# Performance work log

Measured on AMD Instinct MI355X. Metric: run time of the kernel, lower is better.

## Reference

```python
import jax, jax.numpy as jnp
import numpy as np

HID, NH_FULL, K, GAMMA = 768, 12, 9, 2
HD = HID // NH_FULL            # 64
NH = NH_FULL // GAMMA          # 6
RH = HD * NH                   # 384 reduced hidden dim
OUT_HALF = HID // 2            # 384
B, S = 8, 1024


def setup_inputs() -> dict:
    key0 = jax.random.key(0)
    ks = jax.random.split(key0, 20)
    r = lambda i, shape, sc=0.02: (jax.random.normal(ks[i], shape, dtype=jnp.float32) * sc)
    inp = {
        'query': jax.random.normal(ks[0], (B, S, HID), dtype=jnp.float32),
        'mask': jnp.ones((B, 1, 1, S), dtype=jnp.int32),
        # q/k/v projections: hidden -> reduced
        'Wq': r(1, (HID, RH)), 'bq': jnp.zeros((RH,), jnp.float32),
        'Wk': r(2, (HID, RH)), 'bk': jnp.zeros((RH,), jnp.float32),
        'Wv': r(3, (HID, RH)), 'bv': jnp.zeros((RH,), jnp.float32),
        # depthwise separable conv: depthwise [HID,1,K] + pointwise [RH,HID]
        'dw_w': r(4, (HID, 1, K), 0.1), 'dw_b': jnp.zeros((HID,), jnp.float32),
        'pw_w': r(5, (RH, HID)), 'pw_b': jnp.zeros((RH,), jnp.float32),
        # self-attn output proj: reduced -> hidden//2
        'Wsa': r(6, (RH, OUT_HALF)), 'bsa': jnp.zeros((OUT_HALF,), jnp.float32),
        # dynamic kernel layer: reduced -> K*NH
        'Wdk': r(7, (RH, K * NH)), 'bdk': jnp.zeros((K * NH,), jnp.float32),
        # dynamic attn output proj: reduced -> hidden//2
        'Wda': r(8, (RH, OUT_HALF)), 'bda': jnp.zeros((OUT_HALF,), jnp.float32),
    }
    # self_attn=True requires query==key==value
    inp['key'] = inp['query']
    inp['value'] = inp['query']
    return inp


def _forward(query, key, value, mask, Wq, bq, Wk, bk, Wv, bv,
             dw_w, dw_b, pw_w, pw_b, Wsa, bsa, Wdk, bdk, Wda, bda):
    b, s, _ = query.shape
    q = query @ Wq + bq          # [B,S,RH]
    k = key @ Wk + bk
    v = value @ Wv + bv

    # ---- depthwise separable conv over key (seq axis), 'same' padding ----
    key_t = jnp.transpose(key, (0, 2, 1))  # [B,HID,S]
    dw = jax.lax.conv_general_dilated(
        key_t, dw_w, window_strides=(1,), padding=[(K // 2, K // 2)],
        feature_group_count=HID, dimension_numbers=('NCH', 'OIH', 'NCH'))
    dw = dw + dw_b[None, :, None]          # [B,HID,S]
    ks_feat = jnp.einsum('bhs,rh->bsr', dw, pw_w) + pw_b  # [B,S,RH]

    # ---- standard multi-head self-attention branch ----
    def split(x):  # [B,S,RH] -> [B,NH,S,HD]
        return x.reshape(b, s, NH, HD).transpose(0, 2, 1, 3)
    qh, kh, vh = split(q), split(k), split(v)
    scores = jnp.einsum('bhqd,bhkd->bhqk', qh, kh) / jnp.sqrt(jnp.float32(HD))
    scores = jnp.where(mask == 0, jnp.float32(-jnp.inf), scores)
    attn_wts = jax.nn.softmax(scores, axis=-1)             # [B,NH,S,S]
    attn_out = jnp.einsum('bhqk,bhkd->bhqd', attn_wts, vh)
    attn_out = attn_out.transpose(0, 2, 1, 3).reshape(b, s, RH)
    self_out = attn_out @ Wsa + bsa                         # [B,S,HID//2]

    # ---- span dynamic conv attention branch ----
    # unfold v into sliding windows: expanded[b,s,h,d,k] = v_pad[b, s+k, h*HD+d]
    v_pad = jnp.pad(v, ((0, 0), (K // 2, K // 2), (0, 0)))  # [B,S+K-1,RH]
    windows = jnp.stack([v_pad[:, i:i + s] for i in range(K)], axis=-1)  # [B,S,RH,K]
    windows = windows.reshape(b, s, NH, HD, K)
    dyn_logits = (q * ks_feat) @ Wdk + bdk                  # [B,S,K*NH]
    dyn_kernel = jax.nn.softmax(dyn_logits.reshape(b, s, NH, K), axis=-1)
    dyn_out = jnp.einsum('bshdk,bshk->bshd', windows, dyn_kernel).reshape(b, s, RH)
    dyn_out = dyn_out @ Wda + bda                           # [B,S,HID//2]

    return attn_wts, jnp.concatenate([self_out, dyn_out], axis=-1)


def reference(query, key, value, mask, Wq, bq, Wk, bk, Wv, bv,
              dw_w, dw_b, pw_w, pw_b, Wsa, bsa, Wdk, bdk, Wda, bda):
    return _forward(query, key, value, mask, Wq, bq, Wk, bk, Wv, bv,
                    dw_w, dw_b, pw_w, pw_b, Wsa, bsa, Wdk, bdk, Wda, bda)
```

## Files before the change

kernel.cpp:

```cpp
#include <hip/hip_runtime.h>
#include <math.h>

#define B 8
#define S 1024
#define HID 768
#define RH 384
#define NH 6
#define HD 64
#define KW 9
#define KNH 54
#define OUTHALF 384
#define QLD 1152
#define EXPSCALE 0.18033688f

typedef __attribute__((ext_vector_type(8))) short short8;
typedef __attribute__((ext_vector_type(4))) float f32x4;

#define SWZ(r, c) (((r) << 6) + ((c) ^ (((r) & 7) << 3)))

__device__ __forceinline__ ushort f2bf(float x) {
    unsigned u = __float_as_uint(x);
    u += 0x7FFF + ((u >> 16) & 1);
    return (ushort)(u >> 16);
}
__device__ __forceinline__ float bf2f(ushort u) {
    return __uint_as_float(((unsigned)u) << 16);
}
__device__ __forceinline__ short8 cvt8(const float* p) {
    short8 r;
    #pragma unroll
    for (int i = 0; i < 8; i++) r[i] = (short)f2bf(p[i]);
    return r;
}

__device__ __forceinline__ void gld16(const ushort* g, ushort* l) {
    __builtin_amdgcn_global_load_lds(
        (const __attribute__((address_space(1))) void*)g,
        (__attribute__((address_space(3))) void*)l,
        16, 0, 0);
}

__global__ __launch_bounds__(256) void cvt_dw_fused(
    const float* __restrict__ query, const float* __restrict__ dw_w,
    const float* __restrict__ dw_b, ushort* __restrict__ Xbf,
    ushort* __restrict__ dwout)
{
    int idx = blockIdx.x*256 + threadIdx.x;
    if (idx >= B*S*(HID/8)) return;
    int c0 = (idx % (HID/8))*8;
    int s  = (idx / (HID/8)) % S;
    int b  = idx / ((HID/8)*S);

    float ctr[8];
    *(float4*)&ctr[0] = *(const float4*)(query + ((size_t)b*S + s)*HID + c0);
    *(float4*)&ctr[4] = *(const float4*)(query + ((size_t)b*S + s)*HID + c0 + 4);
    *(short8*)(Xbf + ((size_t)b*S + s)*HID + c0) = cvt8(ctr);

    float acc[8];
    *(float4*)&acc[0] = *(const float4*)(dw_b + c0);
    *(float4*)&acc[4] = *(const float4*)(dw_b + c0 + 4);
    #pragma unroll
    for (int kk = 0; kk < KW; kk++) {
        int sp = s + kk - KW/2;
        if (sp >= 0 && sp < S) {
            float row[8];
            *(float4*)&row[0] = *(const float4*)(query + ((size_t)b*S + sp)*HID + c0);
            *(float4*)&row[4] = *(const float4*)(query + ((size_t)b*S + sp)*HID + c0 + 4);
            #pragma unroll
            for (int j = 0; j < 8; j++)
                acc[j] += row[j] * dw_w[(c0+j)*KW + kk];
        }
    }
    *(short8*)(dwout + ((size_t)b*S + s)*HID + c0) = cvt8(acc);
}

__global__ __launch_bounds__(256) void prep_weights(
    const float* __restrict__ Wq, const float* __restrict__ Wk, const float* __restrict__ Wv,
    const float* __restrict__ bq, const float* __restrict__ bk, const float* __restrict__ bv,
    const float* __restrict__ pw_w, const float* __restrict__ Wsa,
    const float* __restrict__ Wda, const float* __restrict__ Wdk,
    ushort* __restrict__ WqkvT, ushort* __restrict__ pw_bf,
    ushort* __restrict__ WsaT, ushort* __restrict__ WdaT, ushort* __restrict__ WdkT,
    float* __restrict__ bqkv)
{
    int i = blockIdx.x*256 + threadIdx.x;
    if (i < 884736) {
        int n = i / 768, kk = i % 768;
        int w = n / 384, nn = n % 384;
        const float* W = (w == 0) ? Wq : (w == 1) ? Wk : Wv;
        WqkvT[i] = f2bf(W[kk*384 + nn]);
        return;
    }
    i -= 884736;
    if (i < 294912) { pw_bf[i] = f2bf(pw_w[i]); return; }
    i -= 294912;
    if (i < 147456) {
        int n = i / 384, kk = i % 384;
        WsaT[i] = f2bf(Wsa[kk*384 + n]);
        return;
    }
    i -= 147456;
    if (i < 147456) {
        int n = i / 384, kk = i % 384;
        WdaT[i] = f2bf(Wda[kk*384 + n]);
        return;
    }
    i -= 147456;
    if (i < 49152) {
        int n = i / 384, kk = i % 384;
        WdkT[i] = (n < KNH) ? f2bf(Wdk[kk*KNH + n]) : (ushort)0;
        return;
    }
    i -= 49152;
    if (i < 1152) {
        bqkv[i] = (i < 384) ? bq[i] : (i < 768) ? bk[i-384] : bv[i-768];
    }
}

template<bool OUTBF>
__global__ __launch_bounds__(256) void gemm_mfma(
    const ushort* __restrict__ A, const ushort* __restrict__ Bt,
    const float* __restrict__ bias, void* __restrict__ Cout,
    int N, int Kd, int ldc)
{
    __shared__ __attribute__((aligned(16))) ushort As[128*32];
    __shared__ __attribute__((aligned(16))) ushort Bs[128*32];
    const int t = threadIdx.x;
    const int wave = t >> 6, lane = t & 63;
    const int lr = lane & 15, lg = lane >> 4;
    const int wr = wave >> 1, wc = wave & 1;
    const int bm = blockIdx.y * 128, bn = blockIdx.x * 128;

    f32x4 acc[4][4] = {};
    const int srow = t >> 2, sseg = t & 3;
    const int cs = sseg ^ (srow & 3);
    const int swz = lg ^ (lr & 3);

    const ushort* Asrc0 = A + (size_t)(bm + srow)*Kd + cs*8;
    const ushort* Asrc1 = A + (size_t)(bm + 64 + srow)*Kd + cs*8;
    const ushort* Bsrc0 = Bt + (size_t)(bn + srow)*Kd + cs*8;
    const ushort* Bsrc1 = Bt + (size_t)(bn + 64 + srow)*Kd + cs*8;
    ushort* Adst0 = &As[srow*32 + sseg*8];
    ushort* Adst1 = &As[(64 + srow)*32 + sseg*8];
    ushort* Bdst0 = &Bs[srow*32 + sseg*8];
    ushort* Bdst1 = &Bs[(64 + srow)*32 + sseg*8];

    for (int k0 = 0; k0 < Kd; k0 += 32) {
        gld16(Asrc0 + k0, Adst0);
        gld16(Asrc1 + k0, Adst1);
        gld16(Bsrc0 + k0, Bdst0);
        gld16(Bsrc1 + k0, Bdst1);
        __syncthreads();
        short8 af[4], bfr[4];
        #pragma unroll
        for (int m = 0; m < 4; m++)
            af[m] = *(const short8*)&As[(wr*64 + m*16 + lr)*32 + swz*8];
        #pragma unroll
        for (int n = 0; n < 4; n++)
            bfr[n] = *(const short8*)&Bs[(wc*64 + n*16 + lr)*32 + swz*8];
        #pragma unroll
        for (int m = 0; m < 4; m++)
            #pragma unroll
            for (int n = 0; n < 4; n++)
                acc[m][n] = __builtin_amdgcn_mfma_f32_16x16x32_bf16(af[m], bfr[n], acc[m][n], 0, 0, 0);
        __syncthreads();
    }

    #pragma unroll
    for (int m = 0; m < 4; m++) {
        #pragma unroll
        for (int n = 0; n < 4; n++) {
            int gcol = bn + wc*64 + n*16 + lr;
            if (gcol >= N) continue;
            float bz = bias[gcol];
            #pragma unroll
            for (int r = 0; r < 4; r++) {
                size_t grow = bm + wr*64 + m*16 + lg*4 + r;
                float val = acc[m][n][r] + bz;
                if (OUTBF) ((ushort*)Cout)[grow*ldc + gcol] = f2bf(val);
                else       ((float*)Cout)[grow*ldc + gcol] = val;
            }
        }
    }
}

template<bool OUTBF, bool DUAL>
__global__ __launch_bounds__(256) void gemm64(
    const ushort* __restrict__ A0, const ushort* __restrict__ Bt0,
    const float* __restrict__ bias0, void* __restrict__ C0,
    const ushort* __restrict__ A1, const ushort* __restrict__ Bt1,
    const float* __restrict__ bias1,
    int N, int Kd, int ldc)
{
    __shared__ __attribute__((aligned(16))) ushort As[64*32];
    __shared__ __attribute__((aligned(16))) ushort Bs[64*32];
    const ushort* A  = (DUAL && blockIdx.z) ? A1 : A0;
    const ushort* Bt = (DUAL && blockIdx.z) ? Bt1 : Bt0;
    const float* bias = (DUAL && blockIdx.z) ? bias1 : bias0;
    const int coff = (DUAL && blockIdx.z) ? OUTHALF : 0;

    const int t = threadIdx.x;
    const int wave = t >> 6, lane = t & 63;
    const int lr = lane & 15, lg = lane >> 4;
    const int wr = wave >> 1, wc = wave & 1;
    const int bm = blockIdx.y * 64, bn = blockIdx.x * 64;

    f32x4 acc[2][2] = {};
    const int srow = t >> 2, sseg = t & 3;
    const int cs = sseg ^ (srow & 3);
    const int swz = lg ^ (lr & 3);
    const ushort* Asrc = A + (size_t)(bm + srow)*Kd + cs*8;
    const ushort* Bsrc = Bt + (size_t)(bn + srow)*Kd + cs*8;
    ushort* Adst = &As[srow*32 + sseg*8];
    ushort* Bdst = &Bs[srow*32 + sseg*8];

    for (int k0 = 0; k0 < Kd; k0 += 32) {
        gld16(Asrc + k0, Adst);
        gld16(Bsrc + k0, Bdst);
        __syncthreads();
        short8 af[2], bfr[2];
        #pragma unroll
        for (int m = 0; m < 2; m++)
            af[m] = *(const short8*)&As[(wr*32 + m*16 + lr)*32 + swz*8];
        #pragma unroll
        for (int n = 0; n < 2; n++)
            bfr[n] = *(const short8*)&Bs[(wc*32 + n*16 + lr)*32 + swz*8];
        #pragma unroll
        for (int m = 0; m < 2; m++)
            #pragma unroll
            for (int n = 0; n < 2; n++)
                acc[m][n] = __builtin_amdgcn_mfma_f32_16x16x32_bf16(af[m], bfr[n], acc[m][n], 0, 0, 0);
        __syncthreads();
    }

    #pragma unroll
    for (int m = 0; m < 2; m++) {
        #pragma unroll
        for (int n = 0; n < 2; n++) {
            int gcol = bn + wc*32 + n*16 + lr;
            if (gcol >= N) continue;
            float bz = bias[gcol];
            #pragma unroll
            for (int r = 0; r < 4; r++) {
                size_t grow = bm + wr*32 + m*16 + lg*4 + r;
                float val = acc[m][n][r] + bz;
                if (OUTBF) ((ushort*)C0)[grow*ldc + gcol + coff] = f2bf(val);
                else       ((float*)C0)[grow*ldc + gcol + coff] = val;
            }
        }
    }
}

__global__ __launch_bounds__(64) void gemm_qksdk(
    const ushort* __restrict__ qkv, const ushort* __restrict__ ksf,
    const ushort* __restrict__ WdkT, const float* __restrict__ bdk,
    float* __restrict__ dynlog)
{
    const int lane = threadIdx.x;
    const int lr = lane & 15, lg = lane >> 4;
    const int r0 = blockIdx.x * 16;
    const int row = r0 + lr;

    f32x4 acc[4] = {};
    for (int ks = 0; ks < RH/32; ks++) {
        int k0 = ks*32 + lg*8;
        short8 qv = *(const short8*)(qkv + (size_t)row*QLD + k0);
        short8 kv = *(const short8*)(ksf + (size_t)row*RH + k0);
        short8 afr;
        #pragma unroll
        for (int j = 0; j < 8; j++)
            afr[j] = (short)f2bf(bf2f((ushort)qv[j]) * bf2f((ushort)kv[j]));
        #pragma unroll
        for (int t4 = 0; t4 < 4; t4++) {
            short8 bfr = *(const short8*)(WdkT + (size_t)(t4*16 + lr)*RH + k0);
            acc[t4] = __builtin_amdgcn_mfma_f32_16x16x32_bf16(afr, bfr, acc[t4], 0, 0, 0);
        }
    }
    #pragma unroll
    for (int t4 = 0; t4 < 4; t4++) {
        int n = t4*16 + lr;
        if (n >= KNH) continue;
        float bz = bdk[n];
        #pragma unroll
        for (int r = 0; r < 4; r++)
            dynlog[(size_t)(r0 + lg*4 + r)*KNH + n] = acc[t4][r] + bz;
    }
}

__global__ __launch_bounds__(256) void attn_scores(
    const ushort* __restrict__ qkv, const int* __restrict__ mask,
    ushort* __restrict__ Praw, float* __restrict__ invbuf)
{
    __shared__ __attribute__((aligned(16))) ushort Ks[2][64*64];
    __shared__ __attribute__((aligned(16))) ushort Ps[4][16*64];

    const int b = blockIdx.z, h = blockIdx.y, q0 = blockIdx.x * 64;
    const int t = threadIdx.x;
    const int wave = t >> 6, lane = t & 63;
    const int lr = lane & 15, lg = lane >> 4;

    const ushort* qrow = qkv + (size_t)(b*S + q0 + wave*16 + lr)*QLD + h*HD;
    short8 aQ0 = *(const short8*)(qrow + lg*8);
    short8 aQ1 = *(const short8*)(qrow + 32 + lg*8);

    const int srow = t >> 2, sseg = t & 3;
    const int* mrow = mask + b*S;
    const ushort* krbase = qkv + RH + (size_t)(b*S + srow)*QLD + h*HD + sseg*16;
    ushort* Psw = &Ps[wave][0];
    const size_t prow0 = (size_t)(b*NH + h)*S + q0 + wave*16;

    float lsum[4] = {0.f, 0.f, 0.f, 0.f};

    {
        short8 k0v = *(const short8*)(krbase);
        short8 k1v = *(const short8*)(krbase + 8);
        *(short8*)&Ks[0][SWZ(srow, sseg*16)]     = k0v;
        *(short8*)&Ks[0][SWZ(srow, sseg*16 + 8)] = k1v;
    }
    __syncthreads();
    int cur = 0;

    for (int kc = 0; kc < S; kc += 64) {
        short8 nk0, nk1;
        if (kc + 64 < S) {
            const ushort* kr = krbase + (size_t)(kc + 64)*QLD;
            nk0 = *(const short8*)(kr);
            nk1 = *(const short8*)(kr + 8);
        }
        #pragma unroll
        for (int t4 = 0; t4 < 4; t4++) {
            short8 b0 = *(const short8*)&Ks[cur][SWZ(t4*16 + lr, lg*8)];
            short8 b1 = *(const short8*)&Ks[cur][SWZ(t4*16 + lr, 32 + lg*8)];
            f32x4 c = {0.f, 0.f, 0.f, 0.f};
            c = __builtin_amdgcn_mfma_f32_16x16x32_bf16(aQ0, b0, c, 0, 0, 0);
            c = __builtin_amdgcn_mfma_f32_16x16x32_bf16(aQ1, b1, c, 0, 0, 0);
            float add = mrow[kc + t4*16 + lr] ? 0.f : -1e30f;
            #pragma unroll
            for (int r = 0; r < 4; r++) {
                float p = exp2f(c[r]*EXPSCALE + add);
                lsum[r] += p;
                Psw[SWZ(lg*4 + r, t4*16 + lr)] = f2bf(p);
            }
        }
        {
            int row = lane & 15, seg = lane >> 4;
            short8 p0 = *(const short8*)&Psw[SWZ(row, seg*16)];
            short8 p1 = *(const short8*)&Psw[SWZ(row, seg*16 + 8)];
            ushort* gp = Praw + (prow0 + row)*S + kc + seg*16;
            *(short8*)gp       = p0;
            *(short8*)(gp + 8) = p1;
        }
        if (kc + 64 < S) {
            *(short8*)&Ks[cur^1][SWZ(srow, sseg*16)]     = nk0;
            *(short8*)&Ks[cur^1][SWZ(srow, sseg*16 + 8)] = nk1;
        }
        __syncthreads();
        cur ^= 1;
    }

    #pragma unroll
    for (int r = 0; r < 4; r++) {
        #pragma unroll
        for (int off = 1; off < 16; off <<= 1)
            lsum[r] += __shfl_xor(lsum[r], off, 16);
    }
    if (lr == 0) {
        #pragma unroll
        for (int r = 0; r < 4; r++)
            invbuf[prow0 + lg*4 + r] = 1.f / lsum[r];
    }
}

__global__ __launch_bounds__(256) void attn_pv(
    const ushort* __restrict__ qkv, const ushort* __restrict__ Praw,
    const float* __restrict__ invbuf, float* __restrict__ out0,
    ushort* __restrict__ attnbf)
{
    __shared__ __attribute__((aligned(16))) ushort Pt[2][64*64];
    __shared__ __attribute__((aligned(16))) ushort Vt[2][64*64];

    const int b = blockIdx.z, h = blockIdx.y, q0 = blockIdx.x * 64;
    const int t = threadIdx.x;
    const int wave = t >> 6, lane = t & 63;
    const int lr = lane & 15, lg = lane >> 4;
    const int srow = t >> 2, sseg = t & 3;

    const size_t rbase = (size_t)(b*NH + h)*S + q0;
    const ushort* prbase = Praw + (rbase + srow)*S + sseg*16;
    const ushort* vbase  = qkv + 2*RH + (size_t)b*S*QLD + h*HD + srow;

    const float inv_c = invbuf[rbase + wave*16 + lr];
    float inv_o[4];
    #pragma unroll
    for (int r = 0; r < 4; r++) inv_o[r] = invbuf[rbase + wave*16 + lg*4 + r];

    {
        short8 p0 = *(const short8*)(prbase);
        short8 p1 = *(const short8*)(prbase + 8);
        ushort vb[16];
        #pragma unroll
        for (int i = 0; i < 16; i++)
            vb[i] = vbase[(size_t)(sseg*16 + i)*QLD];
        *(short8*)&Pt[0][SWZ(srow, sseg*16)]     = p0;
        *(short8*)&Pt[0][SWZ(srow, sseg*16 + 8)] = p1;
        *(short8*)&Vt[0][SWZ(srow, sseg*16)]     = *(short8*)&vb[0];
        *(short8*)&Vt[0][SWZ(srow, sseg*16 + 8)] = *(short8*)&vb[8];
    }
    __syncthreads();
    int cur = 0;

    f32x4 o[4] = {};
    const size_t orow = (rbase + wave*16 + lr)*(size_t)S;

    for (int kc = 0; kc < S; kc += 64) {
        short8 np0, np1;
        ushort vb[16];
        if (kc + 64 < S) {
            np0 = *(const short8*)(prbase + kc + 64);
            np1 = *(const short8*)(prbase + kc + 72);
            const ushort* vp = vbase + (size_t)(kc + 64)*QLD;
            #pragma unroll
            for (int i = 0; i < 16; i++)
                vb[i] = vp[(size_t)(sseg*16 + i)*QLD];
        }

        #pragma unroll
        for (int kh = 0; kh < 2; kh++) {
            short8 pa = *(const short8*)&Pt[cur][SWZ(wave*16 + lr, kh*32 + lg*8)];
            float pf[8];
            #pragma unroll
            for (int j = 0; j < 8; j++) pf[j] = bf2f((ushort)pa[j]) * inv_c;
            float* op = out0 + orow + kc + kh*32 + lg*8;
            __builtin_nontemporal_store(*(f32x4*)&pf[0], (f32x4*)op);
            __builtin_nontemporal_store(*(f32x4*)&pf[4], (f32x4*)(op + 4));
            #pragma unroll
            for (int dt = 0; dt < 4; dt++) {
                short8 vv = *(const short8*)&Vt[cur][SWZ(dt*16 + lr, kh*32 + lg*8)];
                o[dt] = __builtin_amdgcn_mfma_f32_16x16x32_bf16(pa, vv, o[dt], 0, 0, 0);
            }
        }

        if (kc + 64 < S) {
            *(short8*)&Pt[cur^1][SWZ(srow, sseg*16)]     = np0;
            *(short8*)&Pt[cur^1][SWZ(srow, sseg*16 + 8)] = np1;
            *(short8*)&Vt[cur^1][SWZ(srow, sseg*16)]     = *(short8*)&vb[0];
            *(short8*)&Vt[cur^1][SWZ(srow, sseg*16 + 8)] = *(short8*)&vb[8];
        }
        __syncthreads();
        cur ^= 1;
    }

    #pragma unroll
    for (int dt = 0; dt < 4; dt++)
        #pragma unroll
        for (int r = 0; r < 4; r++)
            attnbf[(size_t)(b*S + q0 + wave*16 + lg*4 + r)*RH + h*HD + dt*16 + lr] =
                f2bf(o[dt][r] * inv_o[r]);
}

__global__ __launch_bounds__(256) void dyn_conv(
    const float* __restrict__ logits, const ushort* __restrict__ qkv,
    ushort* __restrict__ dynout)
{
    int idx = blockIdx.x*256 + threadIdx.x;
    if (idx >= B*S*(RH/4)) return;
    int r4 = (idx % (RH/4))*4;
    int s  = (idx / (RH/4)) % S;
    int b  = idx / ((RH/4)*S);
    int h  = r4 / HD;
    const float* lg = logits + ((size_t)b*S + s)*KNH + h*KW;
    float mx = lg[0];
    #pragma unroll
    for (int kk = 1; kk < KW; kk++) mx = fmaxf(mx, lg[kk]);
    float e[KW], sum = 0.f;
    #pragma unroll
    for (int kk = 0; kk < KW; kk++) { e[kk] = __expf(lg[kk]-mx); sum += e[kk]; }
    float inv = 1.f/sum;
    float acc[4] = {0.f, 0.f, 0.f, 0.f};
    const ushort* vbase = qkv + 2*RH;
    #pragma unroll
    for (int kk = 0; kk < KW; kk++) {
        int sp = s + kk - KW/2;
        if (sp >= 0 && sp < S) {
            const ushort* vp = vbase + (size_t)(b*S + sp)*QLD + r4;
            #pragma unroll
            for (int j = 0; j < 4; j++) acc[j] += bf2f(vp[j]) * e[kk];
        }
    }
    ushort4 o;
    o.x = f2bf(acc[0]*inv); o.y = f2bf(acc[1]*inv);
    o.z = f2bf(acc[2]*inv); o.w = f2bf(acc[3]*inv);
    *(ushort4*)(dynout + ((size_t)b*S + s)*RH + r4) = o;
}

extern "C" void kernel_launch(void* const* d_in, const int* in_sizes, int n_in,
                              void* d_out, int out_size, void* d_ws, size_t ws_size,
                              hipStream_t stream) {
    const float* query = (const float*)d_in[0];
    const int*   mask  = (const int*)d_in[1];
    const float* Wq    = (const float*)d_in[2];
    const float* bq    = (const float*)d_in[3];
    const float* Wk    = (const float*)d_in[4];
    const float* bk    = (const float*)d_in[5];
    const float* Wv    = (const float*)d_in[6];
    const float* bv    = (const float*)d_in[7];
    const float* dw_w  = (const float*)d_in[8];
    const float* dw_b  = (const float*)d_in[9];
    const float* pw_w  = (const float*)d_in[10];
    const float* pw_b  = (const float*)d_in[11];
    const float* Wsa   = (const float*)d_in[12];
    const float* bsa   = (const float*)d_in[13];
    const float* Wdk   = (const float*)d_in[14];
    const float* bdk   = (const float*)d_in[15];
    const float* Wda   = (const float*)d_in[16];
    const float* bda   = (const float*)d_in[17];

    float* out0 = (float*)d_out;
    float* out1 = out0 + (size_t)B*NH*S*S;

    char* wsb = (char*)d_ws;
    size_t off = 0;
    auto alloc = [&](size_t bytes) { char* p = wsb + off; off += (bytes + 255) & ~255ull; return p; };
    ushort* Xbf    = (ushort*)alloc((size_t)B*S*HID*2);
    ushort* qkvbf  = (ushort*)alloc((size_t)B*S*QLD*2);
    ushort* dwbf   = (ushort*)alloc((size_t)B*S*HID*2);
    ushort* ksf    = (ushort*)alloc((size_t)B*S*RH*2);
    ushort* attnbf = (ushort*)alloc((size_t)B*S*RH*2);
    ushort* dynbf  = (ushort*)alloc((size_t)B*S*RH*2);
    float*  dynlog = (float*) alloc((size_t)B*S*KNH*4);
    ushort* WqkvT  = (ushort*)alloc((size_t)QLD*HID*2);
    ushort* pw_bf  = (ushort*)alloc((size_t)RH*HID*2);
    ushort* WsaT   = (ushort*)alloc((size_t)RH*RH*2);
    ushort* WdaT   = (ushort*)alloc((size_t)RH*RH*2);
    ushort* WdkT   = (ushort*)alloc((size_t)128*RH*2);
    float*  bqkv   = (float*) alloc((size_t)QLD*4);
    ushort* Praw   = (ushort*)alloc((size_t)B*NH*S*S*2);
    float*  invbuf = (float*) alloc((size_t)B*NH*S*4);

    const int M = B*S;

    prep_weights<<<(1524864 + 255)/256, 256, 0, stream>>>(
        Wq, Wk, Wv, bq, bk, bv, pw_w, Wsa, Wda, Wdk,
        WqkvT, pw_bf, WsaT, WdaT, WdkT, bqkv);

    cvt_dw_fused<<<(M*(HID/8) + 255)/256, 256, 0, stream>>>(query, dw_w, dw_b, Xbf, dwbf);

    gemm_mfma<true><<<dim3(QLD/128, M/128), 256, 0, stream>>>(
        Xbf, WqkvT, bqkv, qkvbf, QLD, HID, QLD);

    gemm64<true, false><<<dim3(RH/64, M/64), 256, 0, stream>>>(
        dwbf, pw_bf, pw_b, ksf, nullptr, nullptr, nullptr, RH, HID, RH);

    attn_scores<<<dim3(S/64, NH, B), 256, 0, stream>>>(qkvbf, mask, Praw, invbuf);
    attn_pv<<<dim3(S/64, NH, B), 256, 0, stream>>>(qkvbf, Praw, invbuf, out0, attnbf);

    gemm_qksdk<<<M/16, 64, 0, stream>>>(qkvbf, ksf, WdkT, bdk, dynlog);

    dyn_conv<<<(M*(RH/4) + 255)/256, 256, 0, stream>>>(dynlog, qkvbf, dynbf);

    gemm64<false, true><<<dim3(OUTHALF/64, M/64, 2), 256, 0, stream>>>(
        attnbf, WsaT, bsa, out1, dynbf, WdaT, bda, OUTHALF, RH, HID);
}
```

Before: 303.0 us.

## Fuse P·V accumulation into score kernel and split normalization into streaming kernel

The score kernel now also loads V tiles (transposed into LDS) and accumulates unnormalized P·V with MFMA in the same loop, writing the normalized attention output directly. The separate attn_pv kernel is replaced by a simple elementwise streaming kernel that rescales the stored bf16 probabilities into the fp32 attention-weights output. This removes the re-read and re-tiling of P and the strided V gather in the second kernel, in exchange for more LDS use and a scalar transposed LDS write of V per tile.

```diff
diff --git a/kernel.cpp b/kernel.cpp
--- a/kernel.cpp
+++ b/kernel.cpp
@@ -287,11 +287,13 @@
     }
 }
 
-__global__ __launch_bounds__(256) void attn_scores(
+__global__ __launch_bounds__(256) void attn_sv(
     const ushort* __restrict__ qkv, const int* __restrict__ mask,
-    ushort* __restrict__ Praw, float* __restrict__ invbuf)
+    ushort* __restrict__ Praw, float* __restrict__ invbuf,
+    ushort* __restrict__ attnbf)
 {
     __shared__ __attribute__((aligned(16))) ushort Ks[2][64*64];
+    __shared__ __attribute__((aligned(16))) ushort Vs[2][64*64];
     __shared__ __attribute__((aligned(16))) ushort Ps[4][16*64];
 
     const int b = blockIdx.z, h = blockIdx.y, q0 = blockIdx.x * 64;
@@ -305,28 +307,40 @@
 
     const int srow = t >> 2, sseg = t & 3;
     const int* mrow = mask + b*S;
-    const ushort* krbase = qkv + RH + (size_t)(b*S + srow)*QLD + h*HD + sseg*16;
+    const ushort* krbase = qkv + RH   + (size_t)(b*S + srow)*QLD + h*HD + sseg*16;
+    const ushort* vrbase = qkv + 2*RH + (size_t)(b*S + srow)*QLD + h*HD + sseg*16;
     ushort* Psw = &Ps[wave][0];
     const size_t prow0 = (size_t)(b*NH + h)*S + q0 + wave*16;
 
     float lsum[4] = {0.f, 0.f, 0.f, 0.f};
+    f32x4 o[4] = {};
 
     {
         short8 k0v = *(const short8*)(krbase);
         short8 k1v = *(const short8*)(krbase + 8);
         *(short8*)&Ks[0][SWZ(srow, sseg*16)]     = k0v;
         *(short8*)&Ks[0][SWZ(srow, sseg*16 + 8)] = k1v;
+        ushort vb[16];
+        *(short8*)&vb[0] = *(const short8*)(vrbase);
+        *(short8*)&vb[8] = *(const short8*)(vrbase + 8);
+        #pragma unroll
+        for (int i = 0; i < 16; i++)
+            Vs[0][SWZ(sseg*16 + i, srow)] = vb[i];
     }
     __syncthreads();
     int cur = 0;
 
     for (int kc = 0; kc < S; kc += 64) {
-        short8 nk0, nk1;
+        short8 nk0, nk1, nv0, nv1;
         if (kc + 64 < S) {
             const ushort* kr = krbase + (size_t)(kc + 64)*QLD;
             nk0 = *(const short8*)(kr);
             nk1 = *(const short8*)(kr + 8);
-        }
+            const ushort* vr = vrbase + (size_t)(kc + 64)*QLD;
+            nv0 = *(const short8*)(vr);
+            nv1 = *(const short8*)(vr + 8);
+        }
+
         #pragma unroll
         for (int t4 = 0; t4 < 4; t4++) {
             short8 b0 = *(const short8*)&Ks[cur][SWZ(t4*16 + lr, lg*8)];
@@ -350,9 +364,25 @@
             *(short8*)gp       = p0;
             *(short8*)(gp + 8) = p1;
         }
+        #pragma unroll
+        for (int kh = 0; kh < 2; kh++) {
+            short8 pa = *(const short8*)&Psw[SWZ(lr, kh*32 + lg*8)];
+            #pragma unroll
+            for (int dt = 0; dt < 4; dt++) {
+                short8 vv = *(const short8*)&Vs[cur][SWZ(dt*16 + lr, kh*32 + lg*8)];
+                o[dt] = __builtin_amdgcn_mfma_f32_16x16x32_bf16(pa, vv, o[dt], 0, 0, 0);
+            }
+        }
+
         if (kc + 64 < S) {
             *(short8*)&Ks[cur^1][SWZ(srow, sseg*16)]     = nk0;
             *(short8*)&Ks[cur^1][SWZ(srow, sseg*16 + 8)] = nk1;
+            ushort vb[16];
+            *(short8*)&vb[0] = nv0;
+            *(short8*)&vb[8] = nv1;
+            #pragma unroll
+            for (int i = 0; i < 16; i++)
+                Vs[cur^1][SWZ(sseg*16 + i, srow)] = vb[i];
         }
         __syncthreads();
         cur ^= 1;
@@ -364,98 +394,36 @@
         for (int off = 1; off < 16; off <<= 1)
             lsum[r] += __shfl_xor(lsum[r], off, 16);
     }
+    float inv[4];
+    #pragma unroll
+    for (int r = 0; r < 4; r++) inv[r] = 1.f / lsum[r];
     if (lr == 0) {
         #pragma unroll
         for (int r = 0; r < 4; r++)
-            invbuf[prow0 + lg*4 + r] = 1.f / lsum[r];
-    }
-}
-
-__global__ __launch_bounds__(256) void attn_pv(
-    const ushort* __restrict__ qkv, const ushort* __restrict__ Praw,
-    const float* __restrict__ invbuf, float* __restrict__ out0,
-    ushort* __restrict__ attnbf)
-{
-    __shared__ __attribute__((aligned(16))) ushort Pt[2][64*64];
-    __shared__ __attribute__((aligned(16))) ushort Vt[2][64*64];
-
-    const int b = blockIdx.z, h = blockIdx.y, q0 = blockIdx.x * 64;
-    const int t = threadIdx.x;
-    const int wave = t >> 6, lane = t & 63;
-    const int lr = lane & 15, lg = lane >> 4;
-    const int srow = t >> 2, sseg = t & 3;
-
-    const size_t rbase = (size_t)(b*NH + h)*S + q0;
-    const ushort* prbase = Praw + (rbase + srow)*S + sseg*16;
-    const ushort* vbase  = qkv + 2*RH + (size_t)b*S*QLD + h*HD + srow;
-
-    const float inv_c = invbuf[rbase + wave*16 + lr];
-    float inv_o[4];
-    #pragma unroll
-    for (int r = 0; r < 4; r++) inv_o[r] = invbuf[rbase + wave*16 + lg*4 + r];
-
-    {
-        short8 p0 = *(const short8*)(prbase);
-        short8 p1 = *(const short8*)(prbase + 8);
-        ushort vb[16];
-        #pragma unroll
-        for (int i = 0; i < 16; i++)
-            vb[i] = vbase[(size_t)(sseg*16 + i)*QLD];
-        *(short8*)&Pt[0][SWZ(srow, sseg*16)]     = p0;
-        *(short8*)&Pt[0][SWZ(srow, sseg*16 + 8)] = p1;
-        *(short8*)&Vt[0][SWZ(srow, sseg*16)]     = *(short8*)&vb[0];
-        *(short8*)&Vt[0][SWZ(srow, sseg*16 + 8)] = *(short8*)&vb[8];
-    }
-    __syncthreads();
-    int cur = 0;
-
-    f32x4 o[4] = {};
-    const size_t orow = (rbase + wave*16 + lr)*(size_t)S;
-
-    for (int kc = 0; kc < S; kc += 64) {
-        short8 np0, np1;
-        ushort vb[16];
-        if (kc + 64 < S) {
-            np0 = *(const short8*)(prbase + kc + 64);
-            np1 = *(const short8*)(prbase + kc + 72);
-            const ushort* vp = vbase + (size_t)(kc + 64)*QLD;
-            #pragma unroll
-            for (int i = 0; i < 16; i++)
-                vb[i] = vp[(size_t)(sseg*16 + i)*QLD];
-        }
-
-        #pragma unroll
-        for (int kh = 0; kh < 2; kh++) {
-            short8 pa = *(const short8*)&Pt[cur][SWZ(wave*16 + lr, kh*32 + lg*8)];
-            float pf[8];
-            #pragma unroll
-            for (int j = 0; j < 8; j++) pf[j] = bf2f((ushort)pa[j]) * inv_c;
-            float* op = out0 + orow + kc + kh*32 + lg*8;
-            __builtin_nontemporal_store(*(f32x4*)&pf[0], (f32x4*)op);
-            __builtin_nontemporal_store(*(f32x4*)&pf[4], (f32x4*)(op + 4));
-            #pragma unroll
-            for (int dt = 0; dt < 4; dt++) {
-                short8 vv = *(const short8*)&Vt[cur][SWZ(dt*16 + lr, kh*32 + lg*8)];
-                o[dt] = __builtin_amdgcn_mfma_f32_16x16x32_bf16(pa, vv, o[dt], 0, 0, 0);
-            }
-        }
-
-        if (kc + 64 < S) {
-            *(short8*)&Pt[cur^1][SWZ(srow, sseg*16)]     = np0;
-            *(short8*)&Pt[cur^1][SWZ(srow, sseg*16 + 8)] = np1;
-            *(short8*)&Vt[cur^1][SWZ(srow, sseg*16)]     = *(short8*)&vb[0];
-            *(short8*)&Vt[cur^1][SWZ(srow, sseg*16 + 8)] = *(short8*)&vb[8];
-        }
-        __syncthreads();
-        cur ^= 1;
-    }
-
+            invbuf[prow0 + lg*4 + r] = inv[r];
+    }
     #pragma unroll
     for (int dt = 0; dt < 4; dt++)
         #pragma unroll
         for (int r = 0; r < 4; r++)
             attnbf[(size_t)(b*S + q0 + wave*16 + lg*4 + r)*RH + h*HD + dt*16 + lr] =
-                f2bf(o[dt][r] * inv_o[r]);
+                f2bf(o[dt][r] * inv[r]);
+}
+
+__global__ __launch_bounds__(256) void norm_stream(
+    const ushort* __restrict__ Praw, const float* __restrict__ invbuf,
+    float* __restrict__ out0)
+{
+    size_t chunk = (size_t)blockIdx.x*256 + threadIdx.x;
+    size_t row = chunk >> 7;
+    float inv = invbuf[row];
+    short8 pv8 = *(const short8*)(Praw + chunk*8);
+    float pf[8];
+    #pragma unroll
+    for (int j = 0; j < 8; j++) pf[j] = bf2f((ushort)pv8[j]) * inv;
+    float* op = out0 + chunk*8;
+    __builtin_nontemporal_store(*(f32x4*)&pf[0], (f32x4*)op);
+    __builtin_nontemporal_store(*(f32x4*)&pf[4], (f32x4*)(op + 4));
 }
 
 __global__ __launch_bounds__(256) void dyn_conv(
@@ -551,8 +519,8 @@
     gemm64<true, false><<<dim3(RH/64, M/64), 256, 0, stream>>>(
         dwbf, pw_bf, pw_b, ksf, nullptr, nullptr, nullptr, RH, HID, RH);
 
-    attn_scores<<<dim3(S/64, NH, B), 256, 0, stream>>>(qkvbf, mask, Praw, invbuf);
-    attn_pv<<<dim3(S/64, NH, B), 256, 0, stream>>>(qkvbf, Praw, invbuf, out0, attnbf);
+    attn_sv<<<dim3(S/64, NH, B), 256, 0, stream>>>(qkvbf, mask, Praw, invbuf, attnbf);
+    norm_stream<<<(B*NH*S*(S/8))/256, 256, 0, stream>>>(Praw, invbuf, out0);
 
     gemm_qksdk<<<M/16, 64, 0, stream>>>(qkvbf, ksf, WdkT, bdk, dynlog);
 
```

Measured after the change: 319.7 us. 5.5% more time.
